# Optimization experiments

Hardware: AMD Instinct MI355X
Metric: run time of the kernel (lower is better)

The kernel has to match this reference:

```python
import jax, jax.numpy as jnp
import numpy as np

N_NODES = 50000
N_EDGES = 800000
IN_DIM = 128
OUT_DIM = 64
NEG_SLOPE = 0.01  # torch F.leaky_relu default


def setup_inputs() -> dict:
    key = jax.random.key(0)
    ks = jax.random.split(key, 7)
    h = jax.random.normal(ks[0], (N_NODES, IN_DIM), dtype=jnp.float32)
    embed = jax.random.uniform(ks[1], (N_EDGES, 1), dtype=jnp.float32)
    src = jax.random.randint(ks[2], (N_EDGES,), 0, N_NODES)
    dst = jax.random.randint(ks[3], (N_EDGES,), 0, N_NODES)
    # parameters (Linear weights, no bias); stored as [in, out] for x @ W
    W_fc = jax.random.normal(ks[4], (IN_DIM, OUT_DIM), dtype=jnp.float32) / np.sqrt(IN_DIM)
    W_attn = jax.random.normal(ks[5], (3 * OUT_DIM, 1), dtype=jnp.float32) / np.sqrt(3 * OUT_DIM)
    W_feat = jax.random.normal(ks[6], (1, OUT_DIM), dtype=jnp.float32)
    return {"h": h, "embed": embed, "src": src, "dst": dst,
            "W_fc": W_fc, "W_attn": W_attn, "W_feat": W_feat}


def reference(h, embed, src, dst, W_fc, W_attn, W_feat):
    n = h.shape[0]
    z = h @ W_fc                                  # [N, D]
    # split attn weight so we never materialize the [E, 3D] concat
    Wa_src, Wa_dst, Wa_feat = jnp.split(W_attn, 3, axis=0)  # each [D, 1]
    a_src = (z @ Wa_src)[:, 0]                    # [N]
    a_dst = (z @ Wa_dst)[:, 0]                    # [N]
    dfeat = embed @ W_feat                        # [E, D]
    e = a_src[src] + a_dst[dst] + (dfeat @ Wa_feat)[:, 0]  # [E]
    e = jnp.where(e >= 0, e, NEG_SLOPE * e)       # leaky_relu
    # segment softmax over incoming edges of each dst node
    seg_max = jax.ops.segment_max(e, dst, num_segments=n)  # [N]
    ex = jnp.exp(e - seg_max[dst])                # [E]
    denom = jax.ops.segment_sum(ex, dst, num_segments=n)   # [N]
    alpha = ex / denom[dst]                       # [E]
    # weighted scatter-sum of source features
    out = jax.ops.segment_sum(alpha[:, None] * z[src], dst, num_segments=n)  # [N, D]
    return out
```

## Files before the change

### kernel.cpp

```cpp
#include <hip/hip_runtime.h>
#include <hip/hip_fp16.h>

#define N_NODES 50000
#define N_EDGES 800000
#define IN_DIM 128
#define OUT_DIM 64
#define NEG_SLOPE 0.01f

#define BUCK_SHIFT 6
#define BUCK_NODES 64
#define NBUCK ((N_NODES + BUCK_NODES - 1) / BUCK_NODES)
#define CAP 1536
#define EPB 3136
#define NBLK_SCAT ((N_EDGES + EPB - 1) / EPB)

typedef unsigned int uint;

__device__ __forceinline__ uint f2h(float x) {
    return (uint)__half_as_ushort(__float2half_rn(x));
}
__device__ __forceinline__ float h2f(unsigned short u) {
    return __half2float(__ushort_as_half(u));
}

__launch_bounds__(256)
__global__ void k_fc(const float* __restrict__ h,
                     const float* __restrict__ W_fc,
                     const float* __restrict__ W_attn,
                     const float* __restrict__ W_feat,
                     uint* __restrict__ z16, float* __restrict__ a_src, float* __restrict__ a_dst,
                     int* __restrict__ gcursor, float* __restrict__ c_ws) {
    __shared__ float Wlds[IN_DIM * OUT_DIM];
    const float4* Wg = (const float4*)W_fc;
    float4* Wl = (float4*)Wlds;
    #pragma unroll
    for (int i = 0; i < 8; ++i) Wl[threadIdx.x + i * 256] = Wg[threadIdx.x + i * 256];

    int g = blockIdx.x * 256 + threadIdx.x;
    if (g < NBUCK) gcursor[g] = g * CAP;
    if (blockIdx.x == 0 && threadIdx.x < 64) {
        int lane = threadIdx.x;
        float p = W_feat[lane] * W_attn[128 + lane];
        #pragma unroll
        for (int off = 32; off; off >>= 1) p += __shfl_xor(p, off, 64);
        if (lane == 0) c_ws[0] = p;
    }
    __syncthreads();

    int quad = g >> 4;
    int og   = g & 15;
    int n0 = quad * 4;
    if (n0 >= N_NODES) return;

    bool valid[4];
    const float4* hrow[4];
    #pragma unroll
    for (int i = 0; i < 4; ++i) {
        int n = n0 + i;
        valid[i] = (n < N_NODES);
        hrow[i] = (const float4*)(h + (size_t)(valid[i] ? n : (N_NODES - 1)) * IN_DIM);
    }

    float acc[4][4];
    #pragma unroll
    for (int i = 0; i < 4; ++i)
        #pragma unroll
        for (int d = 0; d < 4; ++d) acc[i][d] = 0.f;

    for (int kc = 0; kc < IN_DIM / 4; ++kc) {
        float4 hv[4];
        #pragma unroll
        for (int i = 0; i < 4; ++i) hv[i] = hrow[i][kc];
        #pragma unroll
        for (int j = 0; j < 4; ++j) {
            float4 wv = *(const float4*)(Wlds + (size_t)(kc * 4 + j) * OUT_DIM + og * 4);
            #pragma unroll
            for (int i = 0; i < 4; ++i) {
                float hh = (j == 0) ? hv[i].x : (j == 1) ? hv[i].y : (j == 2) ? hv[i].z : hv[i].w;
                acc[i][0] += hh * wv.x;
                acc[i][1] += hh * wv.y;
                acc[i][2] += hh * wv.z;
                acc[i][3] += hh * wv.w;
            }
        }
    }

    #pragma unroll
    for (int i = 0; i < 4; ++i) {
        if (!valid[i]) continue;
        uint* zr = z16 + (size_t)(n0 + i) * (OUT_DIM / 2) + og * 2;
        zr[0] = f2h(acc[i][0]) | (f2h(acc[i][1]) << 16);
        zr[1] = f2h(acc[i][2]) | (f2h(acc[i][3]) << 16);
    }

    float was0 = W_attn[og * 4], was1 = W_attn[og * 4 + 1],
          was2 = W_attn[og * 4 + 2], was3 = W_attn[og * 4 + 3];
    float wad0 = W_attn[64 + og * 4], wad1 = W_attn[64 + og * 4 + 1],
          wad2 = W_attn[64 + og * 4 + 2], wad3 = W_attn[64 + og * 4 + 3];
    #pragma unroll
    for (int i = 0; i < 4; ++i) {
        float ps = acc[i][0] * was0 + acc[i][1] * was1 + acc[i][2] * was2 + acc[i][3] * was3;
        float pd = acc[i][0] * wad0 + acc[i][1] * wad1 + acc[i][2] * wad2 + acc[i][3] * wad3;
        ps += __shfl_xor(ps, 1, 64); ps += __shfl_xor(ps, 2, 64);
        ps += __shfl_xor(ps, 4, 64); ps += __shfl_xor(ps, 8, 64);
        pd += __shfl_xor(pd, 1, 64); pd += __shfl_xor(pd, 2, 64);
        pd += __shfl_xor(pd, 4, 64); pd += __shfl_xor(pd, 8, 64);
        if (og == 0 && valid[i]) { a_src[n0 + i] = ps; a_dst[n0 + i] = pd; }
    }
}

__launch_bounds__(1024)
__global__ void k_binscat(const int* __restrict__ src, const int* __restrict__ dst,
                          const float* __restrict__ embed,
                          const float* __restrict__ a_src,
                          const float* __restrict__ c_ws,
                          int* __restrict__ gcursor, uint2* __restrict__ entries) {
    __shared__ uint2 s_ent[EPB];
    __shared__ int hist[NBUCK];
    __shared__ int boff[NBUCK];
    int t = threadIdx.x;
    if (t < NBUCK) hist[t] = 0;
    __syncthreads();

    int e0 = blockIdx.x * EPB;
    int e1 = e0 + EPB; if (e1 > N_EDGES) e1 = N_EDGES;
    int m = e1 - e0;
    if (m <= 0) return;
    float cc = c_ws[0];

    int i0 = t * 4;
    if (i0 + 3 < m) {
        int4   s4 = ((const int4*)(src + e0))[t];
        int4   d4 = ((const int4*)(dst + e0))[t];
        float4 m4 = ((const float4*)(embed + e0))[t];
        int    ss[4] = {s4.x, s4.y, s4.z, s4.w};
        int    dd[4] = {d4.x, d4.y, d4.z, d4.w};
        float  mm[4] = {m4.x, m4.y, m4.z, m4.w};
        #pragma unroll
        for (int u = 0; u < 4; ++u) {
            float partial = a_src[ss[u]] + cc * mm[u];
            uint b = (uint)dd[u] >> BUCK_SHIFT, dl = (uint)dd[u] & (BUCK_NODES - 1);
            s_ent[i0 + u] = make_uint2((uint)ss[u] | (dl << 16) | (b << 22),
                                       __float_as_uint(partial));
            atomicAdd(&hist[b], 1);
        }
    } else {
        for (int i = i0; i < m; ++i) {
            int e = e0 + i;
            int s = src[e], d = dst[e];
            float partial = a_src[s] + cc * embed[e];
            uint b = (uint)d >> BUCK_SHIFT, dl = (uint)d & (BUCK_NODES - 1);
            s_ent[i] = make_uint2((uint)s | (dl << 16) | (b << 22),
                                  __float_as_uint(partial));
            atomicAdd(&hist[b], 1);
        }
    }
    __syncthreads();

    if (t < NBUCK) {
        int c = hist[t];
        boff[t] = c ? atomicAdd(&gcursor[t], c) : 0;
        hist[t] = 0;
    }
    __syncthreads();

    for (int i = t; i < m; i += 1024) {
        uint2 p = s_ent[i];
        uint b = p.x >> 22;
        int pos = boff[b] + atomicAdd(&hist[b], 1);
        entries[pos] = make_uint2(p.x & 0x3FFFFFu, p.y);
    }
}

__launch_bounds__(1024)
__global__ void k_gather(const int* __restrict__ gcursor, const uint2* __restrict__ entries,
                         const float* __restrict__ a_dst,
                         const uint* __restrict__ z16, float* __restrict__ out) {
    __shared__ uint2 s_stash[CAP];
    __shared__ uint  s_pk2[CAP];
    __shared__ float s_adst[BUCK_NODES];
    __shared__ int hist[BUCK_NODES], hoff[BUCK_NODES], hcur[BUCK_NODES];

    int b = blockIdx.x;
    int t = threadIdx.x, lane = t & 63, wid = t >> 6;
    int base = b * CAP;
    int m = gcursor[b] - base;
    if (m > CAP) m = CAP;

    if (t < BUCK_NODES) {
        hist[t] = 0;
        int n = b * BUCK_NODES + t;
        s_adst[t] = (n < N_NODES) ? a_dst[n] : 0.f;
    }
    __syncthreads();

    for (int i = t; i < m; i += 1024) {
        uint2 p = entries[base + i];
        s_stash[i] = p;
        atomicAdd(&hist[(p.x >> 16) & 63], 1);
    }
    __syncthreads();

    if (wid == 0) {
        int v = hist[lane], sc = v;
        #pragma unroll
        for (int off = 1; off < 64; off <<= 1) {
            int u = __shfl_up(sc, off, 64);
            if (lane >= off) sc += u;
        }
        hoff[lane] = sc - v;
        hcur[lane] = sc - v;
    }
    __syncthreads();

    for (int i = t; i < m; i += 1024) {
        uint2 p = s_stash[i];
        int dl = (p.x >> 16) & 63;
        float ev = __uint_as_float(p.y) + s_adst[dl];
        ev = (ev >= 0.f) ? ev : NEG_SLOPE * ev;
        float ex = __expf(ev);
        int pos = atomicAdd(&hcur[dl], 1);
        s_pk2[pos] = (p.x & 0xFFFFu) | (f2h(ex) << 16);
    }
    __syncthreads();

    int half = lane >> 5, dp = lane & 31;
    for (int k = 0; k < 4; ++k) {
        int dl = wid * 4 + k;
        int n = b * BUCK_NODES + dl;
        if (n >= N_NODES) continue;
        int j0 = hoff[dl], c = hist[dl], j1 = j0 + c;
        float accx = 0.f, accy = 0.f, den = 0.f;
        for (int j = j0; j < j1; j += 16) {
            uint pk[8];
            #pragma unroll
            for (int u = 0; u < 8; ++u) {
                int idx = j + 8 * half + u;
                int idc = (idx < j1) ? idx : (j1 - 1);
                pk[u] = s_pk2[idc];
                if (idx >= j1) pk[u] &= 0xFFFFu;
            }
            uint zv[8];
            #pragma unroll
            for (int u = 0; u < 8; ++u) zv[u] = z16[(size_t)(pk[u] & 0xFFFFu) * 32 + dp];
            #pragma unroll
            for (int u = 0; u < 8; ++u) {
                float ex = h2f((unsigned short)(pk[u] >> 16));
                den  += ex;
                accx += ex * h2f((unsigned short)(zv[u] & 0xFFFFu));
                accy += ex * h2f((unsigned short)(zv[u] >> 16));
            }
        }
        accx += __shfl_xor(accx, 32, 64);
        accy += __shfl_xor(accy, 32, 64);
        den  += __shfl_xor(den, 32, 64);
        if (lane < 32) {
            float2 r = (c > 0) ? make_float2(accx / den, accy / den) : make_float2(0.f, 0.f);
            ((float2*)(out + (size_t)n * OUT_DIM))[dp] = r;
        }
    }
}

extern "C" void kernel_launch(void* const* d_in, const int* in_sizes, int n_in,
                              void* d_out, int out_size, void* d_ws, size_t ws_size,
                              hipStream_t stream) {
    const float* h      = (const float*)d_in[0];
    const float* embed  = (const float*)d_in[1];
    const int*   src    = (const int*)d_in[2];
    const int*   dst    = (const int*)d_in[3];
    const float* W_fc   = (const float*)d_in[4];
    const float* W_attn = (const float*)d_in[5];
    const float* W_feat = (const float*)d_in[6];

    float* ws      = (float*)d_ws;
    uint*  z16     = (uint*)ws;
    uint2* entries = (uint2*)(z16 + (size_t)N_NODES * 32);
    float* a_src   = (float*)(entries + (size_t)NBUCK * CAP);
    float* a_dst   = a_src + N_NODES;
    float* c_ws    = a_dst + N_NODES;
    int*   gcursor = (int*)(c_ws + 1);

    float* out = (float*)d_out;

    k_fc<<<(N_NODES * 4 + 255) / 256, 256, 0, stream>>>(h, W_fc, W_attn, W_feat,
                                                        z16, a_src, a_dst, gcursor, c_ws);
    k_binscat<<<NBLK_SCAT, 1024, 0, stream>>>(src, dst, embed, a_src, c_ws,
                                              gcursor, entries);
    k_gather<<<NBUCK, 1024, 0, stream>>>(gcursor, entries, a_dst, z16, out);
}
```

Before: 70.29 us.

## Double bucket size, keep binned entries in registers, halve gather block threads

Buckets now cover 128 destination nodes instead of 64, which halves the bucket count and the number of global cursor atomics and gather blocks. The scatter kernel now holds each thread's four entries in registers instead of staging them through a shared-memory array, freeing LDS and raising occupancy for the binning pass. The gather kernel runs with 512 threads, each wave handling 16 nodes, and its scan is rewritten to cover two nodes per lane. Larger buckets mean larger per-block shared buffers in the gather kernel and more sequential node work per wave, which may reduce latency hiding.

Result: slower. 75.60 us (+7.6%).

```diff
diff --git a/kernel.cpp b/kernel.cpp
--- a/kernel.cpp
+++ b/kernel.cpp
@@ -7,10 +7,10 @@
 #define OUT_DIM 64
 #define NEG_SLOPE 0.01f
 
-#define BUCK_SHIFT 6
-#define BUCK_NODES 64
+#define BUCK_SHIFT 7
+#define BUCK_NODES 128
 #define NBUCK ((N_NODES + BUCK_NODES - 1) / BUCK_NODES)
-#define CAP 1536
+#define CAP 3072
 #define EPB 3136
 #define NBLK_SCAT ((N_EDGES + EPB - 1) / EPB)
 
@@ -115,7 +115,6 @@
                           const float* __restrict__ a_src,
                           const float* __restrict__ c_ws,
                           int* __restrict__ gcursor, uint2* __restrict__ entries) {
-    __shared__ uint2 s_ent[EPB];
     __shared__ int hist[NBUCK];
     __shared__ int boff[NBUCK];
     int t = threadIdx.x;
@@ -125,8 +124,10 @@
     int e0 = blockIdx.x * EPB;
     int e1 = e0 + EPB; if (e1 > N_EDGES) e1 = N_EDGES;
     int m = e1 - e0;
-    if (m <= 0) return;
     float cc = c_ws[0];
+
+    uint keyr[4]; float valr[4];
+    bool own[4] = {false, false, false, false};
 
     int i0 = t * 4;
     if (i0 + 3 < m) {
@@ -138,21 +139,25 @@
         float  mm[4] = {m4.x, m4.y, m4.z, m4.w};
         #pragma unroll
         for (int u = 0; u < 4; ++u) {
-            float partial = a_src[ss[u]] + cc * mm[u];
             uint b = (uint)dd[u] >> BUCK_SHIFT, dl = (uint)dd[u] & (BUCK_NODES - 1);
-            s_ent[i0 + u] = make_uint2((uint)ss[u] | (dl << 16) | (b << 22),
-                                       __float_as_uint(partial));
+            keyr[u] = (uint)ss[u] | (dl << 16) | (b << 23);
+            valr[u] = a_src[ss[u]] + cc * mm[u];
+            own[u] = true;
             atomicAdd(&hist[b], 1);
         }
     } else {
-        for (int i = i0; i < m; ++i) {
-            int e = e0 + i;
-            int s = src[e], d = dst[e];
-            float partial = a_src[s] + cc * embed[e];
-            uint b = (uint)d >> BUCK_SHIFT, dl = (uint)d & (BUCK_NODES - 1);
-            s_ent[i] = make_uint2((uint)s | (dl << 16) | (b << 22),
-                                  __float_as_uint(partial));
-            atomicAdd(&hist[b], 1);
+        #pragma unroll
+        for (int u = 0; u < 4; ++u) {
+            int i = i0 + u;
+            if (i < m) {
+                int e = e0 + i;
+                int s = src[e], d = dst[e];
+                uint b = (uint)d >> BUCK_SHIFT, dl = (uint)d & (BUCK_NODES - 1);
+                keyr[u] = (uint)s | (dl << 16) | (b << 23);
+                valr[u] = a_src[s] + cc * embed[e];
+                own[u] = true;
+                atomicAdd(&hist[b], 1);
+            }
         }
     }
     __syncthreads();
@@ -164,15 +169,16 @@
     }
     __syncthreads();
 
-    for (int i = t; i < m; i += 1024) {
-        uint2 p = s_ent[i];
-        uint b = p.x >> 22;
+    #pragma unroll
+    for (int u = 0; u < 4; ++u) {
+        if (!own[u]) continue;
+        uint b = keyr[u] >> 23;
         int pos = boff[b] + atomicAdd(&hist[b], 1);
-        entries[pos] = make_uint2(p.x & 0x3FFFFFu, p.y);
-    }
-}
-
-__launch_bounds__(1024)
+        entries[pos] = make_uint2(keyr[u] & 0x7FFFFFu, __float_as_uint(valr[u]));
+    }
+}
+
+__launch_bounds__(512)
 __global__ void k_gather(const int* __restrict__ gcursor, const uint2* __restrict__ entries,
                          const float* __restrict__ a_dst,
                          const uint* __restrict__ z16, float* __restrict__ out) {
@@ -194,28 +200,30 @@
     }
     __syncthreads();
 
-    for (int i = t; i < m; i += 1024) {
+    for (int i = t; i < m; i += 512) {
         uint2 p = entries[base + i];
         s_stash[i] = p;
-        atomicAdd(&hist[(p.x >> 16) & 63], 1);
+        atomicAdd(&hist[(p.x >> 16) & 127], 1);
     }
     __syncthreads();
 
     if (wid == 0) {
-        int v = hist[lane], sc = v;
+        int v0 = hist[2 * lane], v1 = hist[2 * lane + 1];
+        int tot = v0 + v1, sc = tot;
         #pragma unroll
         for (int off = 1; off < 64; off <<= 1) {
             int u = __shfl_up(sc, off, 64);
             if (lane >= off) sc += u;
         }
-        hoff[lane] = sc - v;
-        hcur[lane] = sc - v;
-    }
-    __syncthreads();
-
-    for (int i = t; i < m; i += 1024) {
+        int ex = sc - tot;
+        hoff[2 * lane] = ex;       hcur[2 * lane] = ex;
+        hoff[2 * lane + 1] = ex + v0; hcur[2 * lane + 1] = ex + v0;
+    }
+    __syncthreads();
+
+    for (int i = t; i < m; i += 512) {
         uint2 p = s_stash[i];
-        int dl = (p.x >> 16) & 63;
+        int dl = (p.x >> 16) & 127;
         float ev = __uint_as_float(p.y) + s_adst[dl];
         ev = (ev >= 0.f) ? ev : NEG_SLOPE * ev;
         float ex = __expf(ev);
@@ -225,8 +233,8 @@
     __syncthreads();
 
     int half = lane >> 5, dp = lane & 31;
-    for (int k = 0; k < 4; ++k) {
-        int dl = wid * 4 + k;
+    for (int k = 0; k < 16; ++k) {
+        int dl = wid * 16 + k;
         int n = b * BUCK_NODES + dl;
         if (n >= N_NODES) continue;
         int j0 = hoff[dl], c = hist[dl], j1 = j0 + c;
@@ -286,5 +294,5 @@
                                                         z16, a_src, a_dst, gcursor, c_ws);
     k_binscat<<<NBLK_SCAT, 1024, 0, stream>>>(src, dst, embed, a_src, c_ws,
                                               gcursor, entries);
-    k_gather<<<NBUCK, 1024, 0, stream>>>(gcursor, entries, a_dst, z16, out);
-}
+    k_gather<<<NBUCK, 512, 0, stream>>>(gcursor, entries, a_dst, z16, out);
+}
```
